# Kernel optimization log

Measured on AMD Instinct MI355X. Metric: run time of the kernel, lower is better.

Reference implementation:

```python
import jax, jax.numpy as jnp
import numpy as np

N_NODES = 100_000
SCALAR_DIM = 64
HIDDEN = 64
ATTR_DIM = 3
N_DIH = 1_000_000
IN_DIM = SCALAR_DIM * 2 + ATTR_DIM + 2  # 133
EPS_LN = 1e-5
EPS_NORM = 1e-6


def setup_inputs() -> dict:
    key = jax.random.key(0)
    ks = jax.random.split(key, 8)
    x = jax.random.normal(ks[0], (N_NODES, SCALAR_DIM), jnp.float32)
    pos = jax.random.normal(ks[1], (N_NODES, 3), jnp.float32)
    quadra_index = jax.random.randint(ks[2], (4, N_DIH), 0, N_NODES, jnp.int32)
    quadra_attr = jax.random.normal(ks[3], (N_DIH, ATTR_DIM), jnp.float32)

    def lin(k, fi, fo):
        lim = 1.0 / np.sqrt(fi)
        return jax.random.uniform(k, (fi, fo), jnp.float32, -lim, lim)

    return dict(
        x=x, pos=pos, quadra_index=quadra_index, quadra_attr=quadra_attr,
        ln_gamma=jnp.ones((IN_DIM,), jnp.float32),
        ln_beta=jnp.zeros((IN_DIM,), jnp.float32),
        w1=lin(ks[4], IN_DIM, HIDDEN), b1=jnp.zeros((HIDDEN,), jnp.float32),
        w2=lin(ks[5], HIDDEN, HIDDEN), b2=jnp.zeros((HIDDEN,), jnp.float32),
        w3=lin(ks[6], HIDDEN, SCALAR_DIM), b3=jnp.zeros((SCALAR_DIM,), jnp.float32),
        w_out=jax.random.normal(ks[7], (SCALAR_DIM, SCALAR_DIM), jnp.float32),
    )


def _dihedral_cos_sin(pos, i, j, k, l):
    b1 = pos[j] - pos[i]
    b2 = pos[k] - pos[j]
    b3 = pos[l] - pos[k]
    n1 = jnp.cross(b1, b2)
    n2 = jnp.cross(b2, b3)
    n1 = n1 / jnp.maximum(jnp.linalg.norm(n1, axis=-1, keepdims=True), EPS_NORM)
    n2 = n2 / jnp.maximum(jnp.linalg.norm(n2, axis=-1, keepdims=True), EPS_NORM)
    cos_d = jnp.clip(jnp.sum(n1 * n2, axis=-1), -1.0, 1.0)
    b2n = b2 / jnp.maximum(jnp.linalg.norm(b2, axis=-1, keepdims=True), EPS_NORM)
    m = jnp.cross(n1, b2n)
    sin_d = jnp.sum(m * n2, axis=-1)
    return cos_d, sin_d


def _segment_mean(v, idx, n):
    s = jax.ops.segment_sum(v, idx, num_segments=n)
    c = jax.ops.segment_sum(jnp.ones((idx.shape[0], 1), v.dtype), idx, num_segments=n)
    return s / jnp.maximum(c, 1.0)


def reference(x, pos, quadra_index, quadra_attr,
              ln_gamma, ln_beta, w1, b1, w2, b2, w3, b3, w_out):
    i, j, k, l = quadra_index[0], quadra_index[1], quadra_index[2], quadra_index[3]
    x_scalar = x[:, :SCALAR_DIM]
    cos_d, sin_d = _dihedral_cos_sin(pos, i, j, k, l)
    # [num_dihedrals, 2*scalar_dim + 3 + 2]
    inp = jnp.concatenate(
        [x_scalar[i], x_scalar[l], quadra_attr, cos_d[:, None], sin_d[:, None]], axis=-1)
    # LayerNorm over last dim
    mu = jnp.mean(inp, axis=-1, keepdims=True)
    var = jnp.mean(jnp.square(inp - mu), axis=-1, keepdims=True)
    inp = (inp - mu) * jax.lax.rsqrt(var + EPS_LN) * ln_gamma + ln_beta
    # MLP with SiLU
    h = jax.nn.silu(inp @ w1 + b1)
    h = jax.nn.silu(h @ w2 + b2)
    msg = h @ w3 + b3  # [num_dihedrals, scalar_dim]
    aggr = 0.5 * (_segment_mean(msg, j, N_NODES) + _segment_mean(msg, k, N_NODES))
    # e3nn o3.Linear on scalars: fan-in normalized linear, no bias
    out = (aggr @ w_out) * (1.0 / np.sqrt(SCALAR_DIM))
    return out
```

## Files before the change

kernel.cpp:

```cpp
#include <hip/hip_runtime.h>
#include <math.h>

#define NN 100000
#define ND 1000000
#define INDIM 133
#define K1P 160
#define NCNT (2*NN)
#define SCAN_CHUNK 2048
#define NBLK_SCAN ((NCNT + SCAN_CHUNK - 1) / SCAN_CHUNK)
#define HS 72
#define NBLK_X (NN / 4)
#define NBLK_E ((ND + 255) / 256)

typedef __bf16 bf16x8 __attribute__((ext_vector_type(8)));
typedef __bf16 bf16x4 __attribute__((ext_vector_type(4)));
typedef float  f32x4  __attribute__((ext_vector_type(4)));
typedef _Float16 f16;
typedef _Float16 f16x4 __attribute__((ext_vector_type(4)));

__device__ __forceinline__ f32x4 mfma_bf16(bf16x8 a, bf16x8 b, f32x4 c) {
    return __builtin_amdgcn_mfma_f32_16x16x32_bf16(a, b, c, 0, 0, 0);
}

__device__ __forceinline__ float3 f3sub(float3 a, float3 b) {
    return make_float3(a.x - b.x, a.y - b.y, a.z - b.z);
}
__device__ __forceinline__ float3 f3cross(float3 a, float3 b) {
    return make_float3(a.y * b.z - a.z * b.y, a.z * b.x - a.x * b.z, a.x * b.y - a.y * b.x);
}
__device__ __forceinline__ float f3dot(float3 a, float3 b) {
    return a.x * b.x + a.y * b.y + a.z * b.z;
}
__device__ __forceinline__ float3 f3load(const float* __restrict__ p, int idx) {
    const float* q = p + (size_t)idx * 3;
    return make_float3(q[0], q[1], q[2]);
}
__device__ __forceinline__ float fsilu(float v) {
    return v / (1.0f + __expf(-v));
}

__global__ __launch_bounds__(256) void prep_merged(
    const float* __restrict__ x,
    const float* __restrict__ w1, const float* __restrict__ b1,
    const float* __restrict__ w2,
    const float* __restrict__ w3, const float* __restrict__ b3,
    const float* __restrict__ wout,
    const float* __restrict__ gamma, const float* __restrict__ beta,
    const int* __restrict__ qidx,
    __bf16* __restrict__ w1h, __bf16* __restrict__ w1l,
    float* __restrict__ c1, float* __restrict__ d1,
    __bf16* __restrict__ w2h, __bf16* __restrict__ w2l,
    __bf16* __restrict__ w3h, __bf16* __restrict__ w3l,
    float* __restrict__ b3f,
    float2* __restrict__ sq,
    int* __restrict__ cnt)
{
    const int b = blockIdx.x, tid = threadIdx.x;
    if (b < 40) {
        int idx = b * 256 + tid;
        int n = idx / K1P, kp = idx - n * K1P;
        float v = (kp < INDIM) ? gamma[kp] * w1[(size_t)kp * 64 + n] : 0.0f;
        __bf16 h = (__bf16)v;
        w1h[idx] = h;
        w1l[idx] = (__bf16)(v - (float)h);
    } else if (b == 40) {
        if (tid < 64) {
            float sc = 0.0f, sd = 0.0f;
            for (int k = 0; k < INDIM; ++k) {
                float wv = w1[(size_t)k * 64 + tid];
                sc = fmaf(gamma[k], wv, sc);
                sd = fmaf(beta[k], wv, sd);
            }
            c1[tid] = sc;
            d1[tid] = sd + b1[tid];
        }
    } else if (b < 57) {
        int idx = (b - 41) * 256 + tid;
        int n = idx >> 6, kp = idx & 63;
        int ko = 16 * (kp & 3) + (kp >> 2);
        float v = w2[(size_t)ko * 64 + n];
        __bf16 h = (__bf16)v;
        w2h[idx] = h;
        w2l[idx] = (__bf16)(v - (float)h);
    } else if (b == 57) {
        for (int idx = tid; idx < 64 * 64; idx += 256) {
            int k = idx >> 6, c = idx & 63;
            float s = 0.0f;
            for (int q = 0; q < 64; ++q)
                s = fmaf(w3[(size_t)k * 64 + q], wout[(size_t)q * 64 + c], s);
            s *= 0.0625f;
            __bf16 h = (__bf16)s;
            int kp = 4 * (k & 15) + (k >> 4);
            w3h[(size_t)c * 64 + kp] = h;
            w3l[(size_t)c * 64 + kp] = (__bf16)(s - (float)h);
        }
        if (tid < 64) {
            float s = 0.0f;
            for (int q = 0; q < 64; ++q)
                s = fmaf(b3[q], wout[(size_t)q * 64 + tid], s);
            b3f[tid] = s * 0.0625f;
        }
    } else if (b < 58 + NBLK_X) {
        const int n = (b - 58) * 4 + (tid >> 6);
        const int c = tid & 63;
        float v = x[(size_t)n * 64 + c];
        float s = v, q = v * v;
#pragma unroll
        for (int d = 1; d < 64; d <<= 1) {
            s += __shfl_xor(s, d);
            q += __shfl_xor(q, d);
        }
        if (c == 0) sq[n] = make_float2(s, q);
    } else {
        int e = (b - 58 - NBLK_X) * 256 + tid;
        if (e < ND) {
            atomicAdd(&cnt[qidx[ND + e]], 1);
            atomicAdd(&cnt[NN + qidx[2 * ND + e]], 1);
        }
    }
}

__global__ __launch_bounds__(256) void scan1(int* data, int* __restrict__ bsum) {
    __shared__ int lds[256];
    const int tid = threadIdx.x;
    const int base = blockIdx.x * SCAN_CHUNK + tid * 8;
    int v[8];
    int tsum = 0;
#pragma unroll
    for (int t = 0; t < 8; ++t) {
        v[t] = (base + t < NCNT) ? data[base + t] : 0;
        tsum += v[t];
    }
    lds[tid] = tsum;
    __syncthreads();
    for (int d = 1; d < 256; d <<= 1) {
        int u = 0;
        if (tid >= d) u = lds[tid - d];
        __syncthreads();
        lds[tid] += u;
        __syncthreads();
    }
    if (tid == 255) bsum[blockIdx.x] = lds[255];
    int run = lds[tid] - tsum;
#pragma unroll
    for (int t = 0; t < 8; ++t) {
        if (base + t < NCNT) data[base + t] = run;
        run += v[t];
    }
}

__global__ __launch_bounds__(128) void scan2(int* __restrict__ bsum) {
    __shared__ int lds[128];
    const int t = threadIdx.x;
    int v = (t < NBLK_SCAN) ? bsum[t] : 0;
    lds[t] = v;
    __syncthreads();
    for (int d = 1; d < 128; d <<= 1) {
        int u = (t >= d) ? lds[t - d] : 0;
        __syncthreads();
        lds[t] += u;
        __syncthreads();
    }
    if (t < NBLK_SCAN) bsum[t] = lds[t] - v;
}

__global__ __launch_bounds__(256) void scan3(int* __restrict__ off,
                                             const int* __restrict__ bsum) {
    const int base = blockIdx.x * SCAN_CHUNK + threadIdx.x * 8;
    const int add = bsum[blockIdx.x];
#pragma unroll
    for (int t = 0; t < 8; ++t) {
        int i = base + t;
        if (i < NCNT) off[i] += add;
    }
}

__global__ __launch_bounds__(256, 3) void edge_mlp_mfma(
    const float* __restrict__ x,
    const float2* __restrict__ sq,
    const float* __restrict__ pos,
    const int* __restrict__ qidx, const float* __restrict__ qattr,
    const __bf16* __restrict__ w1h, const __bf16* __restrict__ w1l,
    const float* __restrict__ c1, const float* __restrict__ d1,
    const __bf16* __restrict__ w2h, const __bf16* __restrict__ w2l, const float* __restrict__ b2,
    const __bf16* __restrict__ w3h, const __bf16* __restrict__ w3l, const float* __restrict__ b3f,
    int* __restrict__ off,
    f16* __restrict__ msg)
{
    __shared__ __align__(16) __bf16 hsh[4][4][16 * HS];

    const int tid = threadIdx.x;
    const int w   = tid >> 6;
    const int l   = tid & 63;
    const int m   = l & 15;
    const int kg  = l >> 4;
    const int ebase = (blockIdx.x * 4 + w) * 64;
    if (ebase >= ND) return;

    int vj, vk;
    {
        const int me = ebase + l;
        vj = atomicAdd(&off[qidx[ND + me]], 1);
        vk = atomicAdd(&off[NN + qidx[2 * ND + me]], 1);
    }

    int iA[4], lA[4];
#pragma unroll
    for (int t = 0; t < 4; ++t) {
        const int e = ebase + 16 * t + m;
        iA[t] = qidx[e];
        lA[t] = qidx[3 * ND + e];
    }

    float cosd, sind, at0, at1, at2, se, qe;
    {
        const int e2 = ebase + 16 * kg + m;
        const int i2 = qidx[e2];
        const int j2 = qidx[ND + e2];
        const int k2 = qidx[2 * ND + e2];
        const int l2 = qidx[3 * ND + e2];
        float3 pi = f3load(pos, i2), pj = f3load(pos, j2);
        float3 pk = f3load(pos, k2), pl = f3load(pos, l2);
        float3 d1v_ = f3sub(pj, pi);
        float3 d2v_ = f3sub(pk, pj);
        float3 d3v_ = f3sub(pl, pk);
        float3 n1 = f3cross(d1v_, d2v_);
        float3 n2 = f3cross(d2v_, d3v_);
        float r1 = 1.0f / fmaxf(sqrtf(f3dot(n1, n1)), 1e-6f);
        n1.x *= r1; n1.y *= r1; n1.z *= r1;
        float r2 = 1.0f / fmaxf(sqrtf(f3dot(n2, n2)), 1e-6f);
        n2.x *= r2; n2.y *= r2; n2.z *= r2;
        cosd = fminf(fmaxf(f3dot(n1, n2), -1.0f), 1.0f);
        float rb = 1.0f / fmaxf(sqrtf(f3dot(d2v_, d2v_)), 1e-6f);
        float3 b2n = make_float3(d2v_.x * rb, d2v_.y * rb, d2v_.z * rb);
        float3 mm = f3cross(n1, b2n);
        sind = f3dot(mm, n2);
        at0 = qattr[(size_t)e2 * 3 + 0];
        at1 = qattr[(size_t)e2 * 3 + 1];
        at2 = qattr[(size_t)e2 * 3 + 2];
        se = at0 + at1 + at2 + cosd + sind;
        qe = at0 * at0 + at1 * at1 + at2 * at2 + cosd * cosd + sind * sind;
    }

    bf16x8 ah4[4], al4[4];
    float rs_[4], mn_[4];
#pragma unroll
    for (int t = 0; t < 4; ++t) {
        const int src = m + 16 * t;
        float u4[8] = {__shfl(at0, src), __shfl(at1, src), __shfl(at2, src),
                       __shfl(cosd, src), __shfl(sind, src), 0.f, 0.f, 0.f};
        float g0 = (kg == 0) ? 1.0f : 0.0f;
#pragma unroll
        for (int j = 0; j < 8; ++j) {
            float v = u4[j] * g0;
            __bf16 h = (__bf16)v;
            ah4[t][j] = h;
            al4[t][j] = (__bf16)(v - (float)h);
        }
        float2 si = sq[iA[t]], sl = sq[lA[t]];
        float S = si.x + sl.x + __shfl(se, src);
        float Q = si.y + sl.y + __shfl(qe, src);
        float mu  = S * (1.0f / INDIM);
        float var = Q * (1.0f / INDIM) - mu * mu;
        float rsv = rsqrtf(fmaxf(var, 0.0f) + 1e-5f);
        rs_[t] = rsv;
        mn_[t] = -mu * rsv;
    }

    f32x4 acc[4][4];
#pragma unroll
    for (int t = 0; t < 4; ++t)
#pragma unroll
        for (int nt = 0; nt < 4; ++nt) acc[t][nt] = (f32x4){0.f, 0.f, 0.f, 0.f};

#pragma unroll
    for (int nt = 0; nt < 4; ++nt) {
        const size_t wb = (size_t)(16 * nt + m) * K1P + 128 + 8 * kg;
        bf16x8 bh = *(const bf16x8*)(w1h + wb);
        bf16x8 bl = *(const bf16x8*)(w1l + wb);
#pragma unroll
        for (int t = 0; t < 4; ++t) {
            acc[t][nt] = mfma_bf16(ah4[t], bh, acc[t][nt]);
            acc[t][nt] = mfma_bf16(al4[t], bh, acc[t][nt]);
            acc[t][nt] = mfma_bf16(ah4[t], bl, acc[t][nt]);
        }
    }

#pragma unroll
    for (int s = 0; s < 4; ++s) {
        const int colo = 32 * (s & 1) + 8 * kg;
        bf16x8 ath[4], atl[4];
#pragma unroll
        for (int t = 0; t < 4; ++t) {
            const int r_ = (s < 2) ? iA[t] : lA[t];
            float vv[8];
            *(float4*)&vv[0] = *(const float4*)(x + (size_t)r_ * 64 + colo);
            *(float4*)&vv[4] = *(const float4*)(x + (size_t)r_ * 64 + colo + 4);
#pragma unroll
            for (int j = 0; j < 8; ++j) {
                float v = vv[j];
                __bf16 h = (__bf16)v;
                ath[t][j] = h;
                atl[t][j] = (__bf16)(v - (float)h);
            }
        }
#pragma unroll
        for (int nt = 0; nt < 4; ++nt) {
            const size_t wb = (size_t)(16 * nt + m) * K1P + 32 * s + 8 * kg;
            bf16x8 bh = *(const bf16x8*)(w1h + wb);
            bf16x8 bl = *(const bf16x8*)(w1l + wb);
#pragma unroll
            for (int t = 0; t < 4; ++t) {
                acc[t][nt] = mfma_bf16(ath[t], bh, acc[t][nt]);
                acc[t][nt] = mfma_bf16(atl[t], bh, acc[t][nt]);
                acc[t][nt] = mfma_bf16(ath[t], bl, acc[t][nt]);
            }
        }
    }

    float c1v[4], d1v[4], b2v[4], b3v[4];
#pragma unroll
    for (int nt = 0; nt < 4; ++nt) {
        c1v[nt] = c1[16 * nt + m];
        d1v[nt] = d1[16 * nt + m];
        b2v[nt] = b2[16 * nt + m];
        b3v[nt] = b3f[16 * nt + m];
    }
#pragma unroll
    for (int t = 0; t < 4; ++t) {
        __bf16* hhw = &hsh[w][t][0];
#pragma unroll
        for (int r = 0; r < 4; ++r) {
            float rse = __shfl(rs_[t], 4 * kg + r);
            float mne = __shfl(mn_[t], 4 * kg + r);
            bf16x4 hv4;
#pragma unroll
            for (int nt = 0; nt < 4; ++nt)
                hv4[nt] = (__bf16)fsilu(fmaf(rse, acc[t][nt][r],
                                        fmaf(mne, c1v[nt], d1v[nt])));
            *(bf16x4*)(hhw + (4 * kg + r) * HS + m * 4) = hv4;
        }
    }

    bf16x8 a2h[4][2];
#pragma unroll
    for (int t = 0; t < 4; ++t)
#pragma unroll
        for (int s = 0; s < 2; ++s)
            a2h[t][s] = *(const bf16x8*)(&hsh[w][t][m * HS + 32 * s + 8 * kg]);
    f32x4 acc2[4][4];
#pragma unroll
    for (int t = 0; t < 4; ++t)
#pragma unroll
        for (int nt = 0; nt < 4; ++nt) acc2[t][nt] = (f32x4){0.f, 0.f, 0.f, 0.f};
#pragma unroll
    for (int s = 0; s < 2; ++s) {
#pragma unroll
        for (int nt = 0; nt < 4; ++nt) {
            const size_t wb = (size_t)(16 * nt + m) * 64 + 32 * s + 8 * kg;
            bf16x8 bh = *(const bf16x8*)(w2h + wb);
            bf16x8 bl = *(const bf16x8*)(w2l + wb);
#pragma unroll
            for (int t = 0; t < 4; ++t) {
                acc2[t][nt] = mfma_bf16(a2h[t][s], bh, acc2[t][nt]);
                acc2[t][nt] = mfma_bf16(a2h[t][s], bl, acc2[t][nt]);
            }
        }
    }
#pragma unroll
    for (int t = 0; t < 4; ++t) {
        __bf16* hhw = &hsh[w][t][0];
#pragma unroll
        for (int r = 0; r < 4; ++r) {
            bf16x4 hv4;
#pragma unroll
            for (int nt = 0; nt < 4; ++nt)
                hv4[nt] = (__bf16)fsilu(acc2[t][nt][r] + b2v[nt]);
            *(bf16x4*)(hhw + (4 * kg + r) * HS + m * 4) = hv4;
        }
    }

    bf16x8 a3h[4][2];
#pragma unroll
    for (int t = 0; t < 4; ++t)
#pragma unroll
        for (int s = 0; s < 2; ++s)
            a3h[t][s] = *(const bf16x8*)(&hsh[w][t][m * HS + 32 * s + 8 * kg]);
    f32x4 acc3[4][4];
#pragma unroll
    for (int t = 0; t < 4; ++t)
#pragma unroll
        for (int nt = 0; nt < 4; ++nt) acc3[t][nt] = (f32x4){0.f, 0.f, 0.f, 0.f};
#pragma unroll
    for (int s = 0; s < 2; ++s) {
#pragma unroll
        for (int nt = 0; nt < 4; ++nt) {
            const size_t wb = (size_t)(16 * nt + m) * 64 + 32 * s + 8 * kg;
            bf16x8 bh = *(const bf16x8*)(w3h + wb);
            bf16x8 bl = *(const bf16x8*)(w3l + wb);
#pragma unroll
            for (int t = 0; t < 4; ++t) {
                acc3[t][nt] = mfma_bf16(a3h[t][s], bh, acc3[t][nt]);
                acc3[t][nt] = mfma_bf16(a3h[t][s], bl, acc3[t][nt]);
            }
        }
    }

#pragma unroll
    for (int t = 0; t < 4; ++t) {
#pragma unroll
        for (int r = 0; r < 4; ++r) {
            f16x4 v;
#pragma unroll
            for (int nt = 0; nt < 4; ++nt)
                v[nt] = (f16)(acc3[t][nt][r] + b3v[nt]);
            const int src = 16 * t + 4 * kg + r;
            const int sjv = __shfl(vj, src);
            const int skv = __shfl(vk, src);
            *(f16x4*)(msg + (size_t)sjv * 64 + m * 4) = v;
            *(f16x4*)(msg + (size_t)skv * 64 + m * 4) = v;
        }
    }
}

__global__ __launch_bounds__(256) void node_out(const f16* __restrict__ msg,
                                                const int* __restrict__ off,
                                                float* __restrict__ out) {
    const int w   = threadIdx.x >> 6;
    const int l   = threadIdx.x & 63;
    const int sub = l >> 4;
    const int m16 = l & 15;
    for (int n = blockIdx.x * 4 + w; n < NN; n += gridDim.x * 4) {
        int ja = (n == 0) ? 0 : off[n - 1];
        int jb = off[n];
        int ka = off[NN + n - 1];
        int kb = off[NN + n];
        float s0 = 0.f, s1 = 0.f, s2 = 0.f, s3 = 0.f;
        float t0 = 0.f, t1 = 0.f, t2 = 0.f, t3 = 0.f;
        for (int p = ja + sub; p < jb; p += 4) {
            f16x4 v = *(const f16x4*)(msg + (size_t)p * 64 + m16 * 4);
            s0 += (float)v[0]; s1 += (float)v[1];
            s2 += (float)v[2]; s3 += (float)v[3];
        }
        for (int p = ka + sub; p < kb; p += 4) {
            f16x4 v = *(const f16x4*)(msg + (size_t)p * 64 + m16 * 4);
            t0 += (float)v[0]; t1 += (float)v[1];
            t2 += (float)v[2]; t3 += (float)v[3];
        }
        s0 += __shfl_xor(s0, 16); s0 += __shfl_xor(s0, 32);
        s1 += __shfl_xor(s1, 16); s1 += __shfl_xor(s1, 32);
        s2 += __shfl_xor(s2, 16); s2 += __shfl_xor(s2, 32);
        s3 += __shfl_xor(s3, 16); s3 += __shfl_xor(s3, 32);
        t0 += __shfl_xor(t0, 16); t0 += __shfl_xor(t0, 32);
        t1 += __shfl_xor(t1, 16); t1 += __shfl_xor(t1, 32);
        t2 += __shfl_xor(t2, 16); t2 += __shfl_xor(t2, 32);
        t3 += __shfl_xor(t3, 16); t3 += __shfl_xor(t3, 32);
        if (sub == 0) {
            float rj = 1.0f / fmaxf((float)(jb - ja), 1.0f);
            float rk = 1.0f / fmaxf((float)(kb - ka), 1.0f);
            float* o = out + (size_t)n * 64;
            o[m16]      = s0 * rj + t0 * rk;
            o[16 + m16] = s1 * rj + t1 * rk;
            o[32 + m16] = s2 * rj + t2 * rk;
            o[48 + m16] = s3 * rj + t3 * rk;
        }
    }
}


extern "C" void kernel_launch(void* const* d_in, const int* in_sizes, int n_in,
                              void* d_out, int out_size, void* d_ws, size_t ws_size,
                              hipStream_t stream) {
    (void)in_sizes; (void)n_in; (void)out_size;

    const float* x     = (const float*)d_in[0];
    const float* pos   = (const float*)d_in[1];
    const int*   qidx  = (const int*)d_in[2];
    const float* qattr = (const float*)d_in[3];
    const float* gamma = (const float*)d_in[4];
    const float* beta  = (const float*)d_in[5];
    const float* w1    = (const float*)d_in[6];
    const float* b1    = (const float*)d_in[7];
    const float* w2    = (const float*)d_in[8];
    const float* b2    = (const float*)d_in[9];
    const float* w3    = (const float*)d_in[10];
    const float* b3    = (const float*)d_in[11];
    const float* w_out = (const float*)d_in[12];
    float* out = (float*)d_out;

    size_t o = 0;
    auto alloc = [&](size_t bytes) { size_t r = o; o = (o + bytes + 255) & ~(size_t)255; return r; };
    char* W = (char*)d_ws;
    f16*    msg    = (f16*)   (W + alloc((size_t)2 * ND * 64 * sizeof(f16)));
    int*    off    = (int*)   (W + alloc((size_t)NCNT * sizeof(int)));
    int*    bsum   = (int*)   (W + alloc((size_t)NBLK_SCAN * sizeof(int)));
    float2* sqt    = (float2*)(W + alloc((size_t)NN * sizeof(float2)));
    __bf16* w1h    = (__bf16*)(W + alloc((size_t)64 * K1P * sizeof(__bf16)));
    __bf16* w1l    = (__bf16*)(W + alloc((size_t)64 * K1P * sizeof(__bf16)));
    __bf16* w2h    = (__bf16*)(W + alloc((size_t)64 * 64 * sizeof(__bf16)));
    __bf16* w2l    = (__bf16*)(W + alloc((size_t)64 * 64 * sizeof(__bf16)));
    __bf16* w3h    = (__bf16*)(W + alloc((size_t)64 * 64 * sizeof(__bf16)));
    __bf16* w3l    = (__bf16*)(W + alloc((size_t)64 * 64 * sizeof(__bf16)));
    float*  c1     = (float*) (W + alloc((size_t)64 * sizeof(float)));
    float*  d1     = (float*) (W + alloc((size_t)64 * sizeof(float)));
    float*  b3f    = (float*) (W + alloc((size_t)64 * sizeof(float)));
    if (ws_size < o) return;

    hipMemsetAsync(off, 0, (size_t)NCNT * sizeof(int), stream);
    prep_merged<<<58 + NBLK_X + NBLK_E, 256, 0, stream>>>(
        x, w1, b1, w2, w3, b3, w_out, gamma, beta, qidx,
        w1h, w1l, c1, d1, w2h, w2l, w3h, w3l, b3f, sqt, off);

    scan1<<<NBLK_SCAN, 256, 0, stream>>>(off, bsum);
    scan2<<<1, 128, 0, stream>>>(bsum);
    scan3<<<NBLK_SCAN, 256, 0, stream>>>(off, bsum);

    edge_mlp_mfma<<<(ND / 64 + 3) / 4, 256, 0, stream>>>(
        x, sqt, pos, qidx, qattr, w1h, w1l, c1, d1,
        w2h, w2l, b2, w3h, w3l, b3f, off, msg);

    node_out<<<4096, 256, 0, stream>>>(msg, off, out);
}
```

Baseline: 487.7 us.

## Replace three-kernel scan with single-block scan and raise MFMA wave priority

The three-pass multi-block prefix scan over the 200k counts is replaced by one 1024-thread block in which each thread scans 200 contiguous elements serially. This removes two kernel launches and their inter-kernel dependencies, but each thread's accesses are strided rather than coalesced and only one CU does the work. Separately, s_setprio is raised around the MFMA loops in the edge MLP kernel so matrix-issuing waves are favoured by the scheduler over load/conversion phases.

```diff
diff --git a/kernel.cpp b/kernel.cpp
--- a/kernel.cpp
+++ b/kernel.cpp
@@ -6,11 +6,10 @@
 #define INDIM 133
 #define K1P 160
 #define NCNT (2*NN)
-#define SCAN_CHUNK 2048
-#define NBLK_SCAN ((NCNT + SCAN_CHUNK - 1) / SCAN_CHUNK)
 #define HS 72
 #define NBLK_X (NN / 4)
 #define NBLK_E ((ND + 255) / 256)
+#define SCAN_PER 200
 
 typedef __bf16 bf16x8 __attribute__((ext_vector_type(8)));
 typedef __bf16 bf16x4 __attribute__((ext_vector_type(4)));
@@ -120,58 +119,31 @@
     }
 }
 
-__global__ __launch_bounds__(256) void scan1(int* data, int* __restrict__ bsum) {
-    __shared__ int lds[256];
+__global__ __launch_bounds__(1024) void scan_all(int* __restrict__ off) {
+    __shared__ int lds[1024];
     const int tid = threadIdx.x;
-    const int base = blockIdx.x * SCAN_CHUNK + tid * 8;
-    int v[8];
+    const int base = tid * SCAN_PER;
     int tsum = 0;
-#pragma unroll
-    for (int t = 0; t < 8; ++t) {
-        v[t] = (base + t < NCNT) ? data[base + t] : 0;
-        tsum += v[t];
+    for (int i = 0; i < SCAN_PER; ++i) {
+        int idx = base + i;
+        if (idx < NCNT) tsum += off[idx];
     }
     lds[tid] = tsum;
     __syncthreads();
-    for (int d = 1; d < 256; d <<= 1) {
-        int u = 0;
-        if (tid >= d) u = lds[tid - d];
+    for (int d = 1; d < 1024; d <<= 1) {
+        int u = (tid >= d) ? lds[tid - d] : 0;
         __syncthreads();
         lds[tid] += u;
         __syncthreads();
     }
-    if (tid == 255) bsum[blockIdx.x] = lds[255];
     int run = lds[tid] - tsum;
-#pragma unroll
-    for (int t = 0; t < 8; ++t) {
-        if (base + t < NCNT) data[base + t] = run;
-        run += v[t];
-    }
-}
-
-__global__ __launch_bounds__(128) void scan2(int* __restrict__ bsum) {
-    __shared__ int lds[128];
-    const int t = threadIdx.x;
-    int v = (t < NBLK_SCAN) ? bsum[t] : 0;
-    lds[t] = v;
-    __syncthreads();
-    for (int d = 1; d < 128; d <<= 1) {
-        int u = (t >= d) ? lds[t - d] : 0;
-        __syncthreads();
-        lds[t] += u;
-        __syncthreads();
-    }
-    if (t < NBLK_SCAN) bsum[t] = lds[t] - v;
-}
-
-__global__ __launch_bounds__(256) void scan3(int* __restrict__ off,
-                                             const int* __restrict__ bsum) {
-    const int base = blockIdx.x * SCAN_CHUNK + threadIdx.x * 8;
-    const int add = bsum[blockIdx.x];
-#pragma unroll
-    for (int t = 0; t < 8; ++t) {
-        int i = base + t;
-        if (i < NCNT) off[i] += add;
+    for (int i = 0; i < SCAN_PER; ++i) {
+        int idx = base + i;
+        if (idx < NCNT) {
+            int v = off[idx];
+            off[idx] = run;
+            run += v;
+        }
     }
 }
 
@@ -273,6 +245,7 @@
 #pragma unroll
         for (int nt = 0; nt < 4; ++nt) acc[t][nt] = (f32x4){0.f, 0.f, 0.f, 0.f};
 
+    __builtin_amdgcn_s_setprio(1);
 #pragma unroll
     for (int nt = 0; nt < 4; ++nt) {
         const size_t wb = (size_t)(16 * nt + m) * K1P + 128 + 8 * kg;
@@ -285,6 +258,7 @@
             acc[t][nt] = mfma_bf16(ah4[t], bl, acc[t][nt]);
         }
     }
+    __builtin_amdgcn_s_setprio(0);
 
 #pragma unroll
     for (int s = 0; s < 4; ++s) {
@@ -304,6 +278,7 @@
                 atl[t][j] = (__bf16)(v - (float)h);
             }
         }
+        __builtin_amdgcn_s_setprio(1);
 #pragma unroll
         for (int nt = 0; nt < 4; ++nt) {
             const size_t wb = (size_t)(16 * nt + m) * K1P + 32 * s + 8 * kg;
@@ -316,6 +291,7 @@
                 acc[t][nt] = mfma_bf16(ath[t], bl, acc[t][nt]);
             }
         }
+        __builtin_amdgcn_s_setprio(0);
     }
 
     float c1v[4], d1v[4], b2v[4], b3v[4];
@@ -353,6 +329,7 @@
     for (int t = 0; t < 4; ++t)
 #pragma unroll
         for (int nt = 0; nt < 4; ++nt) acc2[t][nt] = (f32x4){0.f, 0.f, 0.f, 0.f};
+    __builtin_amdgcn_s_setprio(1);
 #pragma unroll
     for (int s = 0; s < 2; ++s) {
 #pragma unroll
@@ -367,6 +344,7 @@
             }
         }
     }
+    __builtin_amdgcn_s_setprio(0);
 #pragma unroll
     for (int t = 0; t < 4; ++t) {
         __bf16* hhw = &hsh[w][t][0];
@@ -391,6 +369,7 @@
     for (int t = 0; t < 4; ++t)
 #pragma unroll
         for (int nt = 0; nt < 4; ++nt) acc3[t][nt] = (f32x4){0.f, 0.f, 0.f, 0.f};
+    __builtin_amdgcn_s_setprio(1);
 #pragma unroll
     for (int s = 0; s < 2; ++s) {
 #pragma unroll
@@ -405,6 +384,7 @@
             }
         }
     }
+    __builtin_amdgcn_s_setprio(0);
 
 #pragma unroll
     for (int t = 0; t < 4; ++t) {
@@ -493,7 +473,6 @@
     char* W = (char*)d_ws;
     f16*    msg    = (f16*)   (W + alloc((size_t)2 * ND * 64 * sizeof(f16)));
     int*    off    = (int*)   (W + alloc((size_t)NCNT * sizeof(int)));
-    int*    bsum   = (int*)   (W + alloc((size_t)NBLK_SCAN * sizeof(int)));
     float2* sqt    = (float2*)(W + alloc((size_t)NN * sizeof(float2)));
     __bf16* w1h    = (__bf16*)(W + alloc((size_t)64 * K1P * sizeof(__bf16)));
     __bf16* w1l    = (__bf16*)(W + alloc((size_t)64 * K1P * sizeof(__bf16)));
@@ -511,9 +490,7 @@
         x, w1, b1, w2, w3, b3, w_out, gamma, beta, qidx,
         w1h, w1l, c1, d1, w2h, w2l, w3h, w3l, b3f, sqt, off);
 
-    scan1<<<NBLK_SCAN, 256, 0, stream>>>(off, bsum);
-    scan2<<<1, 128, 0, stream>>>(bsum);
-    scan3<<<NBLK_SCAN, 256, 0, stream>>>(off, bsum);
+    scan_all<<<1, 1024, 0, stream>>>(off);
 
     edge_mlp_mfma<<<(ND / 64 + 3) / 4, 256, 0, stream>>>(
         x, sqt, pos, qidx, qattr, w1h, w1l, c1, d1,
```

After: 845.3 us. 1.73x slower.
